# Optimization experiments

Hardware: AMD Instinct MI355X
Metric: run time of the kernel (lower is better)

Reference implementation:

```python
import jax, jax.numpy as jnp
import numpy as np

N_ENT = 50000
N_REL = 237
DIM = 200
BATCH = 1024
N_EDGE_RAW = 400000
WALK_LEN = 3


def _build_graph():
    rng = np.random.default_rng(0)
    src = rng.integers(0, N_ENT, N_EDGE_RAW)
    dst = rng.integers(0, N_ENT, N_EDGE_RAW)
    key = np.unique(src.astype(np.int64) * N_ENT + dst.astype(np.int64))
    row = (key // N_ENT).astype(np.int64)
    col = (key % N_ENT).astype(np.int64)
    # symmetric D^{-1/2} A D^{-1/2} normalization (binary coalesced adjacency)
    deg = np.bincount(row, minlength=N_ENT).astype(np.float64)
    dinv = np.where(deg > 0, deg ** -0.5, 0.0)
    adj_val = (dinv[row] * dinv[col]).astype(np.float32)
    # random walk of length 3 from every node (torch_cluster.random_walk semantics)
    rowptr = np.concatenate([[0], np.cumsum(np.bincount(row, minlength=N_ENT))]).astype(np.int64)
    cur = np.arange(N_ENT)
    walk = [cur]
    for _ in range(WALK_LEN):
        d = rowptr[cur + 1] - rowptr[cur]
        off = np.floor(rng.random(N_ENT) * np.maximum(d, 1)).astype(np.int64)
        idx = np.minimum(rowptr[cur] + off, len(row) - 1)
        nxt = np.where(d > 0, col[idx], cur)
        walk.append(nxt)
        cur = nxt
    walk = np.stack(walk, 1)  # (N, WALK_LEN+1)
    # scatter(rw_adj, 1, walk, 1): binary rows, duplicates collapse; then D^{-1} row-normalize
    rw_key = np.unique(np.repeat(np.arange(N_ENT), WALK_LEN + 1).astype(np.int64) * N_ENT + walk.reshape(-1))
    rw_row = (rw_key // N_ENT).astype(np.int64)
    rw_col = (rw_key % N_ENT).astype(np.int64)
    rw_deg = np.bincount(rw_row, minlength=N_ENT).astype(np.float64)
    rw_val = (1.0 / np.maximum(rw_deg[rw_row], 1.0)).astype(np.float32)
    return row, col, adj_val, rw_row, rw_col, rw_val


def setup_inputs() -> dict:
    row, col, adj_val, rw_row, rw_col, rw_val = _build_graph()
    E = row.shape[0]
    key = jax.random.key(0)
    ks = jax.random.split(key, 12)
    g = 0.05
    return dict(
        entity_emb=jax.random.normal(ks[0], (N_ENT, DIM), jnp.float32) * g,
        rel_emb=jax.random.normal(ks[1], (2 * N_REL, DIM * DIM), jnp.float32) * 0.01,
        node_W1=jax.random.normal(ks[2], (2, DIM, DIM), jnp.float32) * g,
        node_b1=jnp.zeros((2, DIM), jnp.float32),
        node_W2=jax.random.normal(ks[3], (2, DIM, 1), jnp.float32) * g,
        node_b2=jnp.zeros((2, 1), jnp.float32),
        edge_W1=jax.random.normal(ks[4], (2, 2 * DIM, DIM), jnp.float32) * g,
        edge_b1=jnp.zeros((2, DIM), jnp.float32),
        edge_W2=jax.random.normal(ks[5], (2, DIM, 1), jnp.float32) * g,
        edge_b2=jnp.zeros((2, 1), jnp.float32),
        adj_row=jnp.asarray(row), adj_col=jnp.asarray(col), adj_val=jnp.asarray(adj_val),
        rw_row=jnp.asarray(rw_row), rw_col=jnp.asarray(rw_col), rw_val=jnp.asarray(rw_val),
        node_eps=jax.random.uniform(ks[6], (2, N_ENT, 1), jnp.float32),
        edge_eps=jax.random.uniform(ks[7], (2, E, 1), jnp.float32),
        sub=jax.random.randint(ks[8], (BATCH,), 0, N_ENT),
        rel=jax.random.randint(ks[9], (BATCH,), 0, 2 * N_REL),
        obj=jax.random.randint(ks[10], (BATCH,), 0, N_ENT),
        neg_tail=jax.random.randint(ks[11], (BATCH, 2), 0, N_ENT),
    )


def _spmm(row, col, val, x, n):
    # sparse COO (row, col, val) @ dense x, output (n, d)
    return jax.ops.segment_sum(val[:, None] * x[col], row, num_segments=n)


def _gate(logits, u):
    # concrete-gate noise: eps ~ U(bias, 1-bias); sigmoid((logit(eps)+logits)/0.5)
    bias = 1e-4
    eps = (2.0 * bias - 1.0) * u + (1.0 - bias)
    return jax.nn.sigmoid((jnp.log(eps) - jnp.log1p(-eps) + logits) / 0.5)


def reference(entity_emb, rel_emb, node_W1, node_b1, node_W2, node_b2,
              edge_W1, edge_b1, edge_W2, edge_b2,
              adj_row, adj_col, adj_val, rw_row, rw_col, rw_val,
              node_eps, edge_eps, sub, rel, obj, neg_tail):
    n, d = entity_emb.shape
    e0 = entity_emb
    node_masks, edge_masks = [], []
    edge_cat = jnp.concatenate([e0[adj_row], e0[adj_col]], axis=-1)  # (E, 2d)
    for i in range(2):
        h = jax.nn.relu(e0 @ node_W1[i] + node_b1[i])
        node_masks.append(_gate(h @ node_W2[i] + node_b2[i], node_eps[i]))  # (n,1)
        he = jax.nn.relu(edge_cat @ edge_W1[i] + edge_b1[i])
        edge_masks.append(_gate(he @ edge_W2[i] + edge_b2[i], edge_eps[i])[:, 0])  # (E,)
    # node-drop branch: mix self vs random-walk mean-pooled, then GCN propagate
    x_nd = e0
    for i in range(2):
        mp = _spmm(rw_row, rw_col, rw_val, x_nd, n)
        x_nd = node_masks[i] * x_nd + (1.0 - node_masks[i]) * mp
        x_nd = _spmm(adj_row, adj_col, adj_val, x_nd, n)
    # edge-drop branch: rw propagation twice; only the LAST edge mask is applied (as in source)
    x_ed = e0
    new_edge = adj_val
    for i in range(2):
        x_ed = _spmm(rw_row, rw_col, rw_val, x_ed, n)
        new_edge = adj_val * edge_masks[i]
    x_ed = _spmm(adj_row, adj_col, new_edge, x_ed, n)
    # RESCAL scoring against all entities
    lhs1 = e0[sub]                                   # (B, d)
    rel1 = rel_emb[rel].reshape(-1, d, d)            # (B, d, d)
    self_hr = jnp.einsum('bd,bde->be', lhs1, rel1)   # (B, d)
    scores = jax.nn.sigmoid(self_hr @ e0.T)          # (B, n)
    return scores, x_nd, x_ed
```

## Files before the change

### kernel.cpp

```cpp
#include <hip/hip_runtime.h>
#include <math.h>

#define DIMV 200
typedef unsigned short ushort;
typedef unsigned int uint;
typedef __attribute__((ext_vector_type(8))) __bf16  bf16x8;
typedef __attribute__((ext_vector_type(4))) float   f32x4;

static __device__ __forceinline__ int lower_bound(const int* __restrict__ a, int n, int key) {
    int lo = 0, hi = n;
    while (lo < hi) {
        int mid = (lo + hi) >> 1;
        if (a[mid] < key) lo = mid + 1; else hi = mid;
    }
    return lo;
}

static __device__ __forceinline__ float gate_fn(float u, float logit) {
    float ee = fmaf(u, -0.9998f, 0.9999f);
    float g  = (logf(ee) - log1pf(-ee) + logit) * 2.0f;
    return 1.0f / (1.0f + expf(-g));
}

static __device__ __forceinline__ ushort f2bf(float f) {
    unsigned int u = __float_as_uint(f);
    return (ushort)((u + 0x7fffu + ((u >> 16) & 1u)) >> 16);
}
static __device__ __forceinline__ float2 bfp2f(uint u) {
    float2 r;
    r.x = __uint_as_float(u << 16);
    r.y = __uint_as_float(u & 0xffff0000u);
    return r;
}
static __device__ __forceinline__ uint f2bfp(float a, float b) {
    return (uint)f2bf(a) | ((uint)f2bf(b) << 16);
}

static __device__ __forceinline__ void cvt8_store(ushort* dst, const float* src) {
    float4 a = *(const float4*)src;
    float4 b = *(const float4*)(src + 4);
    dst[0] = f2bf(a.x); dst[1] = f2bf(a.y); dst[2] = f2bf(a.z); dst[3] = f2bf(a.w);
    dst[4] = f2bf(b.x); dst[5] = f2bf(b.y); dst[6] = f2bf(b.z); dst[7] = f2bf(b.w);
}
static __device__ __forceinline__ void zero8_store(ushort* dst) {
#pragma unroll
    for (int i = 0; i < 8; i++) dst[i] = 0;
}

__global__ __launch_bounds__(256) void prep_all(
    const float* __restrict__ e0, ushort* __restrict__ e0bf,
    const float* __restrict__ w1e_src, ushort* __restrict__ W1eT,
    const float* __restrict__ w1n_src, ushort* __restrict__ W1nT,
    const int* __restrict__ adj_row, int E, int* __restrict__ rp_adj,
    const int* __restrict__ rw_row, int Erw, int* __restrict__ rp_rw,
    const float* __restrict__ rel_emb, const int* __restrict__ sub,
    const int* __restrict__ rel, ushort* __restrict__ hrbf, int N)
{
    __shared__ float lhs[DIMV];
    int bid = blockIdx.x;
    const int t = threadIdx.x;

    const int NB0 = (N * 28 + 255) >> 8;
    if (bid < NB0) {
        int idx = bid * 256 + t;
        if (idx < N * 28) {
            int n = idx / 28, c = idx % 28;
            ushort* dst = e0bf + (size_t)n * 224 + c * 8;
            if (c < 25) cvt8_store(dst, e0 + (size_t)n * 200 + c * 8);
            else        zero8_store(dst);
        }
        return;
    }
    bid -= NB0;
    if (bid < 364) {
        int idx = bid * 256 + t;
        if (idx < 416 * 224) {
            int n = idx / 224, k = idx % 224;
            float v = 0.f;
            if (k < 200) {
                if (n < 200)      v = w1e_src[k * 200 + n];
                else if (n < 400) v = w1e_src[(k + 200) * 200 + (n - 200)];
            }
            W1eT[idx] = f2bf(v);
        }
        return;
    }
    bid -= 364;
    if (bid < 364) {
        int i = bid / 182;
        int idx = (bid % 182) * 256 + t;
        if (idx < 208 * 224) {
            int n = idx / 224, k = idx % 224;
            float v = (n < 200 && k < 200) ? w1n_src[i * 40000 + k * 200 + n] : 0.f;
            W1nT[(size_t)i * 208 * 224 + idx] = f2bf(v);
        }
        return;
    }
    bid -= 364;
    const int NBr = (N + 256) >> 8;
    if (bid < NBr) {
        int r = bid * 256 + t;
        if (r <= N) rp_adj[r] = lower_bound(adj_row, E, r);
        return;
    }
    bid -= NBr;
    if (bid < NBr) {
        int r = bid * 256 + t;
        if (r <= N) rp_rw[r] = lower_bound(rw_row, Erw, r);
        return;
    }
    bid -= NBr;
    {
        const int b = bid;
        if (t < DIMV) lhs[t] = e0[(size_t)sub[b] * DIMV + t];
        __syncthreads();
        if (t >= 224) return;
        if (t < DIMV) {
            const float* R = rel_emb + (size_t)rel[b] * (DIMV * DIMV);
            float acc = 0.f;
            for (int dd = 0; dd < DIMV; dd++)
                acc = fmaf(lhs[dd], R[dd * DIMV + t], acc);
            hrbf[(size_t)b * 224 + t] = f2bf(acc);
        } else {
            hrbf[(size_t)b * 224 + t] = 0;
        }
    }
}

__global__ __launch_bounds__(256) void fused_mlp(
    const ushort* __restrict__ e0bf, const ushort* __restrict__ W1eT,
    const ushort* __restrict__ W1nT, ushort* __restrict__ Pb,
    const float* __restrict__ nb1, const float* __restrict__ nW2,
    const float* __restrict__ nb2, const float* __restrict__ neps,
    float* __restrict__ node_mask, int N, int GX)
{
    __shared__ __align__(16) ushort As[2][128 * 40];
    __shared__ __align__(16) ushort Bs[2][208 * 40];
    __shared__ float bsh[208], wsh[208];

    const int r8  = blockIdx.x & 7;
    const int rem = blockIdx.x >> 3;
    const int y   = rem & 3;
    const int q4  = rem >> 2;
    const int x   = r8 + 8 * q4;
    if (x >= GX) return;

    const int t    = threadIdx.x;
    const int lane = t & 63;
    const int w    = t >> 6;
    const int q    = lane >> 4;
    const int ln   = lane & 15;
    const int r0   = x * 128;
    const bool edge = (y < 2);
    const int  i    = y - 2;
    const ushort* Wt = edge ? (W1eT + (size_t)y * 208 * 224)
                            : (W1nT + (size_t)i * 208 * 224);

    if (!edge && t < 208) {
        bsh[t] = (t < 200) ? nb1[i * 200 + t] : 0.f;
        wsh[t] = (t < 200) ? nW2[i * 200 + t] : 0.f;
    }

    f32x4 acc[2][13];
#pragma unroll
    for (int mt = 0; mt < 2; mt++)
#pragma unroll
        for (int nt = 0; nt < 13; nt++) {
            acc[mt][nt][0] = 0.f; acc[mt][nt][1] = 0.f;
            acc[mt][nt][2] = 0.f; acc[mt][nt][3] = 0.f;
        }

    auto stageA = [&](int ks, int buf) {
#pragma unroll
        for (int it = 0; it < 2; it++) {
            int f = t + it * 256;
            int m = f >> 2, c4 = f & 3;
            int g = r0 + m;
            ushort* dst = &As[buf][m * 40 + c4 * 8];
            if (g < N) *(bf16x8*)dst = *(const bf16x8*)&e0bf[(size_t)g * 224 + ks * 32 + c4 * 8];
            else       zero8_store(dst);
        }
    };
    auto stageB = [&](int ks, int buf) {
        for (int f = t; f < 832; f += 256) {
            int n = f >> 2, c4 = f & 3;
            *(bf16x8*)&Bs[buf][n * 40 + c4 * 8] =
                *(const bf16x8*)&Wt[(size_t)n * 224 + ks * 32 + c4 * 8];
        }
    };

    stageA(0, 0); stageB(0, 0);
    __syncthreads();

    for (int ks = 0; ks < 7; ks++) {
        int cur = ks & 1;
        if (ks + 1 < 7) { stageA(ks + 1, cur ^ 1); stageB(ks + 1, cur ^ 1); }
        bf16x8 af0 = *(const bf16x8*)&As[cur][(w * 32 + ln) * 40 + q * 8];
        bf16x8 af1 = *(const bf16x8*)&As[cur][(w * 32 + 16 + ln) * 40 + q * 8];
#pragma unroll
        for (int nt = 0; nt < 13; nt++) {
            bf16x8 bf = *(const bf16x8*)&Bs[cur][(nt * 16 + ln) * 40 + q * 8];
            acc[0][nt] = __builtin_amdgcn_mfma_f32_16x16x32_bf16(af0, bf, acc[0][nt], 0, 0, 0);
            acc[1][nt] = __builtin_amdgcn_mfma_f32_16x16x32_bf16(af1, bf, acc[1][nt], 0, 0, 0);
        }
        __syncthreads();
    }

    if (edge) {
#pragma unroll
        for (int mt = 0; mt < 2; mt++) {
            int gm = r0 + w * 32 + mt * 16 + q * 4;
#pragma unroll
            for (int nt = 0; nt < 13; nt++) {
                int gn = y * 208 + nt * 16 + ln;
                if (gn < 400) {
#pragma unroll
                    for (int r = 0; r < 4; r++)
                        if (gm + r < N) Pb[(size_t)(gm + r) * 400 + gn] = f2bf(acc[mt][nt][r]);
                }
            }
        }
    } else {
        float p[2][4];
#pragma unroll
        for (int mt = 0; mt < 2; mt++)
#pragma unroll
            for (int r = 0; r < 4; r++) {
                float s = 0.f;
#pragma unroll
                for (int nt = 0; nt < 13; nt++) {
                    int n = nt * 16 + ln;
                    float h = fmaxf(acc[mt][nt][r] + bsh[n], 0.f);
                    s = fmaf(h, wsh[n], s);
                }
                p[mt][r] = s;
            }
#pragma unroll
        for (int off = 1; off < 16; off <<= 1)
#pragma unroll
            for (int mt = 0; mt < 2; mt++)
#pragma unroll
                for (int r = 0; r < 4; r++)
                    p[mt][r] += __shfl_xor(p[mt][r], off);

        if (ln == 0) {
            float b2v = nb2[i];
            const float* epsi = neps + (size_t)i * N;
            float* outi = node_mask + (size_t)i * N;
#pragma unroll
            for (int mt = 0; mt < 2; mt++)
#pragma unroll
                for (int r = 0; r < 4; r++) {
                    int g = r0 + w * 32 + mt * 16 + q * 4 + r;
                    if (g < N) outi[g] = gate_fn(epsi[g], p[mt][r] + b2v);
                }
        }
    }
}

static __device__ __forceinline__ void spmm_bb_body(
    const uint* __restrict__ x, int xld, const int* __restrict__ rowptr,
    const int* __restrict__ col, const float* __restrict__ val,
    uint* __restrict__ out, int N, int bid, int t)
{
    const int sub = t >> 7;
    const int d2  = t & 127;
    const int r   = bid * 2 + sub;
    if (d2 >= 100 || r >= N) return;
    const int lo = rowptr[r], hi = rowptr[r + 1];
    float a0 = 0.f, a1 = 0.f, b0 = 0.f, b1 = 0.f;
    int e = lo;
    for (; e + 1 < hi; e += 2) {
        float2 xa = bfp2f(x[(size_t)col[e]     * xld + d2]);
        float2 xb = bfp2f(x[(size_t)col[e + 1] * xld + d2]);
        float v0 = val[e], v1 = val[e + 1];
        a0 = fmaf(v0, xa.x, a0); b0 = fmaf(v0, xa.y, b0);
        a1 = fmaf(v1, xb.x, a1); b1 = fmaf(v1, xb.y, b1);
    }
    if (e < hi) {
        float2 xa = bfp2f(x[(size_t)col[e] * xld + d2]);
        a0 = fmaf(val[e], xa.x, a0); b0 = fmaf(val[e], xa.y, b0);
    }
    out[(size_t)r * 100 + d2] = f2bfp(a0 + a1, b0 + b1);
}

__global__ __launch_bounds__(256) void k3_rw1_egate(
    const uint* __restrict__ e0u, const int* __restrict__ rp_rw,
    const int* __restrict__ rw_col, const float* __restrict__ rw_val,
    uint* __restrict__ Tb,
    const uint* __restrict__ P4, const int* __restrict__ rp_adj,
    const int* __restrict__ adj_col,
    const float* __restrict__ b1, const float* __restrict__ W2,
    const float* __restrict__ b2, const float* __restrict__ eps,
    float* __restrict__ edge_mask, int N, int NB_SP)
{
    int bid = blockIdx.x;
    const int t = threadIdx.x;
    if (bid < NB_SP) {
        spmm_bb_body(e0u, 112, rp_rw, rw_col, rw_val, Tb, N, bid, t);
        return;
    }
    bid -= NB_SP;
    const int lane = t & 63;
    const int w    = t >> 6;
    const int gw   = bid * 4 + w;
    const bool act1 = lane < 36;
    const int dA = 2 * lane;
    const int dB = 128 + 2 * lane;
    const float bb0x = b1[dA], bb0y = b1[dA + 1];
    const float ww0x = W2[dA], ww0y = W2[dA + 1];
    const float bb1x = act1 ? b1[dB] : 0.f, bb1y = act1 ? b1[dB + 1] : 0.f;
    const float ww1x = act1 ? W2[dB] : 0.f, ww1y = act1 ? W2[dB + 1] : 0.f;
    const float b2v = b2[0];

    const int r_lo = gw * 2;
    const int r_hi = min(r_lo + 2, N);
    for (int r = r_lo; r < r_hi; r++) {
        const uint* Pr = P4 + (size_t)r * 200;
        float2 a0 = bfp2f(Pr[lane]);
        float2 a1; a1.x = 0.f; a1.y = 0.f;
        if (act1) a1 = bfp2f(Pr[64 + lane]);
        a0.x += bb0x; a0.y += bb0y; a1.x += bb1x; a1.y += bb1y;
        const int lo = rp_adj[r], hi = rp_adj[r + 1];
        int e = lo;
        for (; e + 1 < hi; e += 2) {
            const uint* Pc0 = P4 + (size_t)adj_col[e]     * 200 + 100;
            const uint* Pc1 = P4 + (size_t)adj_col[e + 1] * 200 + 100;
            float2 q00 = bfp2f(Pc0[lane]);
            float2 q10 = bfp2f(Pc1[lane]);
            float2 q01, q11; q01.x = q01.y = q11.x = q11.y = 0.f;
            if (act1) { q01 = bfp2f(Pc0[64 + lane]); q11 = bfp2f(Pc1[64 + lane]); }
            float s0 = fmaxf(a0.x + q00.x, 0.f) * ww0x + fmaxf(a0.y + q00.y, 0.f) * ww0y
                     + fmaxf(a1.x + q01.x, 0.f) * ww1x + fmaxf(a1.y + q01.y, 0.f) * ww1y;
            float s1 = fmaxf(a0.x + q10.x, 0.f) * ww0x + fmaxf(a0.y + q10.y, 0.f) * ww0y
                     + fmaxf(a1.x + q11.x, 0.f) * ww1x + fmaxf(a1.y + q11.y, 0.f) * ww1y;
#pragma unroll
            for (int off = 32; off; off >>= 1) {
                s0 += __shfl_xor(s0, off);
                s1 += __shfl_xor(s1, off);
            }
            if (lane == 0) {
                edge_mask[e]     = gate_fn(eps[e],     s0 + b2v);
                edge_mask[e + 1] = gate_fn(eps[e + 1], s1 + b2v);
            }
        }
        if (e < hi) {
            const uint* Pc0 = P4 + (size_t)adj_col[e] * 200 + 100;
            float2 q00 = bfp2f(Pc0[lane]);
            float2 q01; q01.x = q01.y = 0.f;
            if (act1) q01 = bfp2f(Pc0[64 + lane]);
            float s0 = fmaxf(a0.x + q00.x, 0.f) * ww0x + fmaxf(a0.y + q00.y, 0.f) * ww0y
                     + fmaxf(a1.x + q01.x, 0.f) * ww1x + fmaxf(a1.y + q01.y, 0.f) * ww1y;
#pragma unroll
            for (int off = 32; off; off >>= 1) s0 += __shfl_xor(s0, off);
            if (lane == 0) edge_mask[e] = gate_fn(eps[e], s0 + b2v);
        }
    }
}

__global__ __launch_bounds__(256) void k4_rw2_combine(
    const uint* __restrict__ Tb, const int* __restrict__ rp_rw,
    const int* __restrict__ rw_col, const float* __restrict__ rw_val,
    uint* __restrict__ T2b,
    const float* __restrict__ e0, const float* __restrict__ mask,
    uint* __restrict__ xndb, int N, int NB_SP)
{
    int bid = blockIdx.x;
    const int t = threadIdx.x;
    if (bid < NB_SP) {
        spmm_bb_body(Tb, 100, rp_rw, rw_col, rw_val, T2b, N, bid, t);
        return;
    }
    bid -= NB_SP;
    int idx = bid * 256 + t;
    if (idx >= N * 100) return;
    float m = mask[idx / 100];
    float2 a = ((const float2*)e0)[idx];
    float2 b = bfp2f(Tb[idx]);
    xndb[idx] = f2bfp(fmaf(m, a.x - b.x, b.x), fmaf(m, a.y - b.y, b.y));
}

__global__ __launch_bounds__(256) void spmm_dual_bb(
    const uint* __restrict__ xA, const uint* __restrict__ xB,
    const int* __restrict__ rowptr, const int* __restrict__ col,
    const float* __restrict__ val, const float* __restrict__ emask,
    float* __restrict__ outA, uint* __restrict__ outB, int N)
{
    const int sub = threadIdx.x >> 7;
    const int d2  = threadIdx.x & 127;
    const int r   = blockIdx.x * 2 + sub;
    if (d2 >= 100 || r >= N) return;
    const int lo = rowptr[r], hi = rowptr[r + 1];
    float a0 = 0.f, a1 = 0.f, b0 = 0.f, b1 = 0.f;
    float c0 = 0.f, c1 = 0.f, d0 = 0.f, d1 = 0.f;
    int e = lo;
    for (; e + 1 < hi; e += 2) {
        size_t o0 = (size_t)col[e]     * 100 + d2;
        size_t o1 = (size_t)col[e + 1] * 100 + d2;
        float v0 = val[e], v1 = val[e + 1];
        float vm0 = v0 * emask[e], vm1 = v1 * emask[e + 1];
        float2 xa0 = bfp2f(xA[o0]), xa1 = bfp2f(xA[o1]);
        float2 xb0 = bfp2f(xB[o0]), xb1 = bfp2f(xB[o1]);
        a0 = fmaf(vm0, xa0.x, a0); b0 = fmaf(vm0, xa0.y, b0);
        a1 = fmaf(vm1, xa1.x, a1); b1 = fmaf(vm1, xa1.y, b1);
        c0 = fmaf(v0, xb0.x, c0);  d0 = fmaf(v0, xb0.y, d0);
        c1 = fmaf(v1, xb1.x, c1);  d1 = fmaf(v1, xb1.y, d1);
    }
    if (e < hi) {
        size_t o0 = (size_t)col[e] * 100 + d2;
        float v0 = val[e], vm0 = v0 * emask[e];
        float2 xa0 = bfp2f(xA[o0]);
        float2 xb0 = bfp2f(xB[o0]);
        a0 = fmaf(vm0, xa0.x, a0); b0 = fmaf(vm0, xa0.y, b0);
        c0 = fmaf(v0, xb0.x, c0);  d0 = fmaf(v0, xb0.y, d0);
    }
    float2 oA; oA.x = a0 + a1; oA.y = b0 + b1;
    ((float2*)outA)[(size_t)r * 100 + d2] = oA;
    outB[(size_t)r * 100 + d2] = f2bfp(c0 + c1, d0 + d1);
}

__global__ __launch_bounds__(256) void rw_combine_bb(
    const uint* __restrict__ x, const int* __restrict__ rowptr,
    const int* __restrict__ col, const float* __restrict__ val,
    const float* __restrict__ mask, uint* __restrict__ out, int N)
{
    const int sub = threadIdx.x >> 7;
    const int d2  = threadIdx.x & 127;
    const int r   = blockIdx.x * 2 + sub;
    if (d2 >= 100 || r >= N) return;
    const int lo = rowptr[r], hi = rowptr[r + 1];
    float a0 = 0.f, a1 = 0.f, b0 = 0.f, b1 = 0.f;
    int e = lo;
    for (; e + 1 < hi; e += 2) {
        float2 xa = bfp2f(x[(size_t)col[e]     * 100 + d2]);
        float2 xb = bfp2f(x[(size_t)col[e + 1] * 100 + d2]);
        float v0 = val[e], v1 = val[e + 1];
        a0 = fmaf(v0, xa.x, a0); b0 = fmaf(v0, xa.y, b0);
        a1 = fmaf(v1, xb.x, a1); b1 = fmaf(v1, xb.y, b1);
    }
    if (e < hi) {
        float2 xa = bfp2f(x[(size_t)col[e] * 100 + d2]);
        a0 = fmaf(val[e], xa.x, a0); b0 = fmaf(val[e], xa.y, b0);
    }
    const float m = mask[r];
    float2 xs = bfp2f(x[(size_t)r * 100 + d2]);
    float sx = a0 + a1, sy = b0 + b1;
    out[(size_t)r * 100 + d2] = f2bfp(fmaf(m, xs.x - sx, sx), fmaf(m, xs.y - sy, sy));
}

__global__ __launch_bounds__(256) void spmm_bf32(
    const uint* __restrict__ x, const int* __restrict__ rowptr,
    const int* __restrict__ col, const float* __restrict__ val,
    float* __restrict__ out, int N)
{
    const int sub = threadIdx.x >> 7;
    const int d2  = threadIdx.x & 127;
    const int r   = blockIdx.x * 2 + sub;
    if (d2 >= 100 || r >= N) return;
    const int lo = rowptr[r], hi = rowptr[r + 1];
    float a0 = 0.f, a1 = 0.f, b0 = 0.f, b1 = 0.f;
    int e = lo;
    for (; e + 1 < hi; e += 2) {
        float2 xa = bfp2f(x[(size_t)col[e]     * 100 + d2]);
        float2 xb = bfp2f(x[(size_t)col[e + 1] * 100 + d2]);
        float v0 = val[e], v1 = val[e + 1];
        a0 = fmaf(v0, xa.x, a0); b0 = fmaf(v0, xa.y, b0);
        a1 = fmaf(v1, xb.x, a1); b1 = fmaf(v1, xb.y, b1);
    }
    if (e < hi) {
        float2 xa = bfp2f(x[(size_t)col[e] * 100 + d2]);
        a0 = fmaf(val[e], xa.x, a0); b0 = fmaf(val[e], xa.y, b0);
    }
    float2 o; o.x = a0 + a1; o.y = b0 + b1;
    ((float2*)out)[(size_t)r * 100 + d2] = o;
}

__global__ __launch_bounds__(256) void scores_mfma(
    const ushort* __restrict__ hrbf, const ushort* __restrict__ e0bf,
    float* __restrict__ scores, int Nent, int GX)
{
    __shared__ __align__(16) ushort Bs[2][192 * 40];

    const int r8  = blockIdx.x & 7;
    const int rem = blockIdx.x >> 3;
    const int y   = rem & 7;
    const int q8  = rem >> 3;
    const int x   = r8 + 8 * q8;
    if (x >= GX) return;

    const int t    = threadIdx.x;
    const int lane = t & 63;
    const int w    = t >> 6;
    const int q    = lane >> 4;
    const int ln   = lane & 15;
    const int n0   = x * 192;
    const int b0   = y * 128;
    const int arow = b0 + w * 32 + ln;

    auto stageB = [&](int ks, int buf) {
        for (int f = t; f < 768; f += 256) {
            int n = f >> 2, c4 = f & 3;
            int gn = n0 + n;
            ushort* dst = &Bs[buf][n * 40 + c4 * 8];
            if (gn < Nent) *(bf16x8*)dst = *(const bf16x8*)&e0bf[(size_t)gn * 224 + ks * 32 + c4 * 8];
            else           zero8_store(dst);
        }
    };
    stageB(0, 0);

    f32x4 acc[2][12];
#pragma unroll
    for (int mt = 0; mt < 2; mt++)
#pragma unroll
        for (int nt = 0; nt < 12; nt++) {
            acc[mt][nt][0] = 0.f; acc[mt][nt][1] = 0.f;
            acc[mt][nt][2] = 0.f; acc[mt][nt][3] = 0.f;
        }

    bf16x8 a0 = *(const bf16x8*)&hrbf[(size_t)arow * 224 + q * 8];
    bf16x8 a1 = *(const bf16x8*)&hrbf[(size_t)(arow + 16) * 224 + q * 8];
    __syncthreads();

    for (int ks = 0; ks < 7; ks++) {
        int cur = ks & 1;
        bf16x8 a0n = a0, a1n = a1;
        if (ks + 1 < 7) {
            stageB(ks + 1, cur ^ 1);
            a0n = *(const bf16x8*)&hrbf[(size_t)arow * 224 + (ks + 1) * 32 + q * 8];
            a1n = *(const bf16x8*)&hrbf[(size_t)(arow + 16) * 224 + (ks + 1) * 32 + q * 8];
        }
#pragma unroll
        for (int nt = 0; nt < 12; nt++) {
            bf16x8 bf = *(const bf16x8*)&Bs[cur][(nt * 16 + ln) * 40 + q * 8];
            acc[0][nt] = __builtin_amdgcn_mfma_f32_16x16x32_bf16(a0, bf, acc[0][nt], 0, 0, 0);
            acc[1][nt] = __builtin_amdgcn_mfma_f32_16x16x32_bf16(a1, bf, acc[1][nt], 0, 0, 0);
        }
        __syncthreads();
        a0 = a0n; a1 = a1n;
    }

#pragma unroll
    for (int mt = 0; mt < 2; mt++) {
        int b = b0 + w * 32 + mt * 16 + q * 4;
#pragma unroll
        for (int nt = 0; nt < 12; nt++) {
            int n = n0 + nt * 16 + ln;
            if (n < Nent) {
#pragma unroll
                for (int r = 0; r < 4; r++)
                    scores[(size_t)(b + r) * Nent + n] = 1.f / (1.f + __expf(-acc[mt][nt][r]));
            }
        }
    }
}

extern "C" void kernel_launch(void* const* d_in, const int* in_sizes, int n_in,
                              void* d_out, int out_size, void* d_ws, size_t ws_size,
                              hipStream_t stream)
{
    const float* e0       = (const float*)d_in[0];
    const float* rel_emb  = (const float*)d_in[1];
    const float* node_W1  = (const float*)d_in[2];
    const float* node_b1  = (const float*)d_in[3];
    const float* node_W2  = (const float*)d_in[4];
    const float* node_b2  = (const float*)d_in[5];
    const float* edge_W1  = (const float*)d_in[6];
    const float* edge_b1  = (const float*)d_in[7];
    const float* edge_W2  = (const float*)d_in[8];
    const float* edge_b2  = (const float*)d_in[9];
    const int*   adj_row  = (const int*)d_in[10];
    const int*   adj_col  = (const int*)d_in[11];
    const float* adj_val  = (const float*)d_in[12];
    const int*   rw_row   = (const int*)d_in[13];
    const int*   rw_col   = (const int*)d_in[14];
    const float* rw_val   = (const float*)d_in[15];
    const float* node_eps = (const float*)d_in[16];
    const float* edge_eps = (const float*)d_in[17];
    const int*   sub      = (const int*)d_in[18];
    const int*   rel      = (const int*)d_in[19];

    const int E   = in_sizes[10];
    const int Erw = in_sizes[13];
    const int N   = in_sizes[0] / DIMV;
    const int B   = in_sizes[18];

    ushort* W1eT = (ushort*)d_ws;
    ushort* W1nT = W1eT + 416 * 224;
    ushort* e0bf = W1nT + 2 * 208 * 224;
    ushort* hrbf = e0bf + (size_t)N * 224;
    float*  fb   = (float*)(hrbf + (size_t)B * 224);
    float*  node_mask = fb;
    float*  edge_mask = node_mask + 2 * (size_t)N;
    int*    rp_adj = (int*)(edge_mask + E);
    int*    rp_rw  = rp_adj + (N + 1);

    float* out    = (float*)d_out;
    float* scores = out;
    float* x_nd   = out + (size_t)B * N;
    float* x_ed   = x_nd + (size_t)N * DIMV;
    uint*   Tb   = (uint*)scores;
    uint*   T2b  = Tb   + (size_t)N * 100;
    uint*   xndb = T2b  + (size_t)N * 100;
    uint*   Tnb  = xndb + (size_t)N * 100;
    uint*   Pb   = Tnb  + (size_t)N * 100;

    const int NB_SP = (N + 1) / 2;
    const int NB0   = (N * 28 + 255) / 256;
    const int NBr   = (N + 256) / 256;
    const int prep_blocks = NB0 + 364 + 364 + NBr + NBr + B;
    const int GXg = (N + 127) / 128;
    const int GXs = (N + 191) / 192;

    prep_all<<<prep_blocks, 256, 0, stream>>>(
        e0, e0bf, edge_W1 + 400 * 200, W1eT, node_W1, W1nT,
        adj_row, E, rp_adj, rw_row, Erw, rp_rw,
        rel_emb, sub, rel, hrbf, N);

    fused_mlp<<<32 * ((GXg + 7) / 8), 256, 0, stream>>>(
        e0bf, W1eT, W1nT, (ushort*)Pb,
        node_b1, node_W2, node_b2, node_eps, node_mask, N, GXg);

    k3_rw1_egate<<<NB_SP + (NB_SP + 3) / 4, 256, 0, stream>>>(
        (const uint*)e0bf, rp_rw, rw_col, rw_val, Tb,
        Pb, rp_adj, adj_col,
        edge_b1 + 200, edge_W2 + 200, edge_b2 + 1, edge_eps + (size_t)E,
        edge_mask, N, NB_SP);

    k4_rw2_combine<<<NB_SP + (N * 100 + 255) / 256, 256, 0, stream>>>(
        Tb, rp_rw, rw_col, rw_val, T2b, e0, node_mask, xndb, N, NB_SP);

    spmm_dual_bb<<<NB_SP, 256, 0, stream>>>(
        T2b, xndb, rp_adj, adj_col, adj_val, edge_mask, x_ed, Tnb, N);

    rw_combine_bb<<<NB_SP, 256, 0, stream>>>(
        Tnb, rp_rw, rw_col, rw_val, node_mask + N, T2b, N);

    spmm_bf32<<<NB_SP, 256, 0, stream>>>(T2b, rp_adj, adj_col, adj_val, x_nd, N);

    scores_mfma<<<64 * ((GXs + 7) / 8), 256, 0, stream>>>(
        hrbf, e0bf, scores, N, GXs);
}
```

Before: 936.6 us.

## Fuse sparse propagation stages into one cooperative kernel with grid syncs

Replaces the five separate sparse-stage kernel launches with a single persistent cooperative kernel that loops over virtual blocks and separates stages with grid-wide syncs, keeping the old kernels as a fallback if the cooperative launch fails. The SpMM and edge-gate loops are also unrolled from 2 to 4 edges, with four independent accumulators to expose more memory-level parallelism. The aim is to cut launch gaps and tail effects between dependent stages. In exchange, the grid is capped at occupancy-limited residency, grid.sync adds its own cost, and the wider unroll raises register pressure.

```diff
diff --git a/kernel.cpp b/kernel.cpp
--- a/kernel.cpp
+++ b/kernel.cpp
@@ -1,5 +1,8 @@
 #include <hip/hip_runtime.h>
+#include <hip/hip_cooperative_groups.h>
 #include <math.h>
+
+namespace cg = cooperative_groups;
 
 #define DIMV 200
 typedef unsigned short ushort;
@@ -261,58 +264,153 @@
 static __device__ __forceinline__ void spmm_bb_body(
     const uint* __restrict__ x, int xld, const int* __restrict__ rowptr,
     const int* __restrict__ col, const float* __restrict__ val,
-    uint* __restrict__ out, int N, int bid, int t)
-{
-    const int sub = t >> 7;
-    const int d2  = t & 127;
-    const int r   = bid * 2 + sub;
+    uint* __restrict__ out, int N, int vb, int t)
+{
+    const int half = t >> 7;
+    const int d2   = t & 127;
+    const int r    = vb * 2 + half;
     if (d2 >= 100 || r >= N) return;
     const int lo = rowptr[r], hi = rowptr[r + 1];
-    float a0 = 0.f, a1 = 0.f, b0 = 0.f, b1 = 0.f;
+    float ax0=0.f,ay0=0.f,ax1=0.f,ay1=0.f,ax2=0.f,ay2=0.f,ax3=0.f,ay3=0.f;
     int e = lo;
-    for (; e + 1 < hi; e += 2) {
-        float2 xa = bfp2f(x[(size_t)col[e]     * xld + d2]);
-        float2 xb = bfp2f(x[(size_t)col[e + 1] * xld + d2]);
-        float v0 = val[e], v1 = val[e + 1];
-        a0 = fmaf(v0, xa.x, a0); b0 = fmaf(v0, xa.y, b0);
-        a1 = fmaf(v1, xb.x, a1); b1 = fmaf(v1, xb.y, b1);
-    }
-    if (e < hi) {
-        float2 xa = bfp2f(x[(size_t)col[e] * xld + d2]);
-        a0 = fmaf(val[e], xa.x, a0); b0 = fmaf(val[e], xa.y, b0);
-    }
-    out[(size_t)r * 100 + d2] = f2bfp(a0 + a1, b0 + b1);
-}
-
-__global__ __launch_bounds__(256) void k3_rw1_egate(
-    const uint* __restrict__ e0u, const int* __restrict__ rp_rw,
-    const int* __restrict__ rw_col, const float* __restrict__ rw_val,
-    uint* __restrict__ Tb,
-    const uint* __restrict__ P4, const int* __restrict__ rp_adj,
-    const int* __restrict__ adj_col,
-    const float* __restrict__ b1, const float* __restrict__ W2,
-    const float* __restrict__ b2, const float* __restrict__ eps,
-    float* __restrict__ edge_mask, int N, int NB_SP)
-{
-    int bid = blockIdx.x;
-    const int t = threadIdx.x;
-    if (bid < NB_SP) {
-        spmm_bb_body(e0u, 112, rp_rw, rw_col, rw_val, Tb, N, bid, t);
-        return;
-    }
-    bid -= NB_SP;
+    for (; e + 3 < hi; e += 4) {
+        int c0=col[e], c1=col[e+1], c2=col[e+2], c3=col[e+3];
+        float v0=val[e], v1=val[e+1], v2=val[e+2], v3=val[e+3];
+        float2 f0=bfp2f(x[(size_t)c0*xld+d2]);
+        float2 f1=bfp2f(x[(size_t)c1*xld+d2]);
+        float2 f2=bfp2f(x[(size_t)c2*xld+d2]);
+        float2 f3=bfp2f(x[(size_t)c3*xld+d2]);
+        ax0=fmaf(v0,f0.x,ax0); ay0=fmaf(v0,f0.y,ay0);
+        ax1=fmaf(v1,f1.x,ax1); ay1=fmaf(v1,f1.y,ay1);
+        ax2=fmaf(v2,f2.x,ax2); ay2=fmaf(v2,f2.y,ay2);
+        ax3=fmaf(v3,f3.x,ax3); ay3=fmaf(v3,f3.y,ay3);
+    }
+    for (; e < hi; e++) {
+        float2 f0=bfp2f(x[(size_t)col[e]*xld+d2]);
+        ax0=fmaf(val[e],f0.x,ax0); ay0=fmaf(val[e],f0.y,ay0);
+    }
+    out[(size_t)r*100+d2] = f2bfp((ax0+ax1)+(ax2+ax3), (ay0+ay1)+(ay2+ay3));
+}
+
+static __device__ __forceinline__ void dual_body(
+    const uint* __restrict__ xA, const uint* __restrict__ xB,
+    const int* __restrict__ rowptr, const int* __restrict__ col,
+    const float* __restrict__ val, const float* __restrict__ emask,
+    float* __restrict__ outA, uint* __restrict__ outB, int N, int vb, int t)
+{
+    const int half = t >> 7;
+    const int d2   = t & 127;
+    const int r    = vb * 2 + half;
+    if (d2 >= 100 || r >= N) return;
+    const int lo = rowptr[r], hi = rowptr[r + 1];
+    float ax0=0.f,ay0=0.f,ax1=0.f,ay1=0.f,ax2=0.f,ay2=0.f,ax3=0.f,ay3=0.f;
+    float cx0=0.f,cy0=0.f,cx1=0.f,cy1=0.f,cx2=0.f,cy2=0.f,cx3=0.f,cy3=0.f;
+    int e = lo;
+    for (; e + 3 < hi; e += 4) {
+        size_t o0=(size_t)col[e]*100+d2,   o1=(size_t)col[e+1]*100+d2;
+        size_t o2=(size_t)col[e+2]*100+d2, o3=(size_t)col[e+3]*100+d2;
+        float v0=val[e], v1=val[e+1], v2=val[e+2], v3=val[e+3];
+        float m0=v0*emask[e], m1=v1*emask[e+1], m2=v2*emask[e+2], m3=v3*emask[e+3];
+        float2 a0=bfp2f(xA[o0]), a1=bfp2f(xA[o1]), a2=bfp2f(xA[o2]), a3=bfp2f(xA[o3]);
+        float2 b0=bfp2f(xB[o0]), b1=bfp2f(xB[o1]), b2=bfp2f(xB[o2]), b3=bfp2f(xB[o3]);
+        ax0=fmaf(m0,a0.x,ax0); ay0=fmaf(m0,a0.y,ay0);
+        ax1=fmaf(m1,a1.x,ax1); ay1=fmaf(m1,a1.y,ay1);
+        ax2=fmaf(m2,a2.x,ax2); ay2=fmaf(m2,a2.y,ay2);
+        ax3=fmaf(m3,a3.x,ax3); ay3=fmaf(m3,a3.y,ay3);
+        cx0=fmaf(v0,b0.x,cx0); cy0=fmaf(v0,b0.y,cy0);
+        cx1=fmaf(v1,b1.x,cx1); cy1=fmaf(v1,b1.y,cy1);
+        cx2=fmaf(v2,b2.x,cx2); cy2=fmaf(v2,b2.y,cy2);
+        cx3=fmaf(v3,b3.x,cx3); cy3=fmaf(v3,b3.y,cy3);
+    }
+    for (; e < hi; e++) {
+        size_t o0=(size_t)col[e]*100+d2;
+        float v0=val[e], m0=v0*emask[e];
+        float2 a0=bfp2f(xA[o0]); float2 b0=bfp2f(xB[o0]);
+        ax0=fmaf(m0,a0.x,ax0); ay0=fmaf(m0,a0.y,ay0);
+        cx0=fmaf(v0,b0.x,cx0); cy0=fmaf(v0,b0.y,cy0);
+    }
+    float2 oA; oA.x=(ax0+ax1)+(ax2+ax3); oA.y=(ay0+ay1)+(ay2+ay3);
+    ((float2*)outA)[(size_t)r*100+d2] = oA;
+    outB[(size_t)r*100+d2] = f2bfp((cx0+cx1)+(cx2+cx3), (cy0+cy1)+(cy2+cy3));
+}
+
+static __device__ __forceinline__ void rwcomb_body(
+    const uint* __restrict__ x, const int* __restrict__ rowptr,
+    const int* __restrict__ col, const float* __restrict__ val,
+    const float* __restrict__ mask, uint* __restrict__ out, int N, int vb, int t)
+{
+    const int half = t >> 7;
+    const int d2   = t & 127;
+    const int r    = vb * 2 + half;
+    if (d2 >= 100 || r >= N) return;
+    const int lo = rowptr[r], hi = rowptr[r + 1];
+    float ax0=0.f,ay0=0.f,ax1=0.f,ay1=0.f,ax2=0.f,ay2=0.f,ax3=0.f,ay3=0.f;
+    int e = lo;
+    for (; e + 3 < hi; e += 4) {
+        int c0=col[e], c1=col[e+1], c2=col[e+2], c3=col[e+3];
+        float v0=val[e], v1=val[e+1], v2=val[e+2], v3=val[e+3];
+        float2 f0=bfp2f(x[(size_t)c0*100+d2]);
+        float2 f1=bfp2f(x[(size_t)c1*100+d2]);
+        float2 f2=bfp2f(x[(size_t)c2*100+d2]);
+        float2 f3=bfp2f(x[(size_t)c3*100+d2]);
+        ax0=fmaf(v0,f0.x,ax0); ay0=fmaf(v0,f0.y,ay0);
+        ax1=fmaf(v1,f1.x,ax1); ay1=fmaf(v1,f1.y,ay1);
+        ax2=fmaf(v2,f2.x,ax2); ay2=fmaf(v2,f2.y,ay2);
+        ax3=fmaf(v3,f3.x,ax3); ay3=fmaf(v3,f3.y,ay3);
+    }
+    for (; e < hi; e++) {
+        float2 f0=bfp2f(x[(size_t)col[e]*100+d2]);
+        ax0=fmaf(val[e],f0.x,ax0); ay0=fmaf(val[e],f0.y,ay0);
+    }
+    const float m = mask[r];
+    float2 xs = bfp2f(x[(size_t)r*100+d2]);
+    float sx=(ax0+ax1)+(ax2+ax3), sy=(ay0+ay1)+(ay2+ay3);
+    out[(size_t)r*100+d2] = f2bfp(fmaf(m, xs.x-sx, sx), fmaf(m, xs.y-sy, sy));
+}
+
+static __device__ __forceinline__ void bf32_body(
+    const uint* __restrict__ x, const int* __restrict__ rowptr,
+    const int* __restrict__ col, const float* __restrict__ val,
+    float* __restrict__ out, int N, int vb, int t)
+{
+    const int half = t >> 7;
+    const int d2   = t & 127;
+    const int r    = vb * 2 + half;
+    if (d2 >= 100 || r >= N) return;
+    const int lo = rowptr[r], hi = rowptr[r + 1];
+    float ax0=0.f,ay0=0.f,ax1=0.f,ay1=0.f,ax2=0.f,ay2=0.f,ax3=0.f,ay3=0.f;
+    int e = lo;
+    for (; e + 3 < hi; e += 4) {
+        int c0=col[e], c1=col[e+1], c2=col[e+2], c3=col[e+3];
+        float v0=val[e], v1=val[e+1], v2=val[e+2], v3=val[e+3];
+        float2 f0=bfp2f(x[(size_t)c0*100+d2]);
+        float2 f1=bfp2f(x[(size_t)c1*100+d2]);
+        float2 f2=bfp2f(x[(size_t)c2*100+d2]);
+        float2 f3=bfp2f(x[(size_t)c3*100+d2]);
+        ax0=fmaf(v0,f0.x,ax0); ay0=fmaf(v0,f0.y,ay0);
+        ax1=fmaf(v1,f1.x,ax1); ay1=fmaf(v1,f1.y,ay1);
+        ax2=fmaf(v2,f2.x,ax2); ay2=fmaf(v2,f2.y,ay2);
+        ax3=fmaf(v3,f3.x,ax3); ay3=fmaf(v3,f3.y,ay3);
+    }
+    for (; e < hi; e++) {
+        float2 f0=bfp2f(x[(size_t)col[e]*100+d2]);
+        ax0=fmaf(val[e],f0.x,ax0); ay0=fmaf(val[e],f0.y,ay0);
+    }
+    float2 o; o.x=(ax0+ax1)+(ax2+ax3); o.y=(ay0+ay1)+(ay2+ay3);
+    ((float2*)out)[(size_t)r*100+d2] = o;
+}
+
+static __device__ __forceinline__ void egate_body(
+    int vb, int t, const uint* __restrict__ P4, const int* __restrict__ rp_adj,
+    const int* __restrict__ adj_col, const float* __restrict__ eps,
+    float* __restrict__ edge_mask, int N,
+    float bb0x, float bb0y, float bb1x, float bb1y,
+    float ww0x, float ww0y, float ww1x, float ww1y, float b2v)
+{
     const int lane = t & 63;
     const int w    = t >> 6;
-    const int gw   = bid * 4 + w;
+    const int gw   = vb * 4 + w;
     const bool act1 = lane < 36;
-    const int dA = 2 * lane;
-    const int dB = 128 + 2 * lane;
-    const float bb0x = b1[dA], bb0y = b1[dA + 1];
-    const float ww0x = W2[dA], ww0y = W2[dA + 1];
-    const float bb1x = act1 ? b1[dB] : 0.f, bb1y = act1 ? b1[dB + 1] : 0.f;
-    const float ww1x = act1 ? W2[dB] : 0.f, ww1y = act1 ? W2[dB + 1] : 0.f;
-    const float b2v = b2[0];
-
     const int r_lo = gw * 2;
     const int r_hi = min(r_lo + 2, N);
     for (int r = r_lo; r < r_hi; r++) {
@@ -323,34 +421,44 @@
         a0.x += bb0x; a0.y += bb0y; a1.x += bb1x; a1.y += bb1y;
         const int lo = rp_adj[r], hi = rp_adj[r + 1];
         int e = lo;
-        for (; e + 1 < hi; e += 2) {
-            const uint* Pc0 = P4 + (size_t)adj_col[e]     * 200 + 100;
-            const uint* Pc1 = P4 + (size_t)adj_col[e + 1] * 200 + 100;
-            float2 q00 = bfp2f(Pc0[lane]);
-            float2 q10 = bfp2f(Pc1[lane]);
-            float2 q01, q11; q01.x = q01.y = q11.x = q11.y = 0.f;
-            if (act1) { q01 = bfp2f(Pc0[64 + lane]); q11 = bfp2f(Pc1[64 + lane]); }
-            float s0 = fmaxf(a0.x + q00.x, 0.f) * ww0x + fmaxf(a0.y + q00.y, 0.f) * ww0y
-                     + fmaxf(a1.x + q01.x, 0.f) * ww1x + fmaxf(a1.y + q01.y, 0.f) * ww1y;
-            float s1 = fmaxf(a0.x + q10.x, 0.f) * ww0x + fmaxf(a0.y + q10.y, 0.f) * ww0y
-                     + fmaxf(a1.x + q11.x, 0.f) * ww1x + fmaxf(a1.y + q11.y, 0.f) * ww1y;
+        for (; e + 3 < hi; e += 4) {
+            const uint* c0 = P4 + (size_t)adj_col[e]     * 200 + 100;
+            const uint* c1 = P4 + (size_t)adj_col[e + 1] * 200 + 100;
+            const uint* c2 = P4 + (size_t)adj_col[e + 2] * 200 + 100;
+            const uint* c3 = P4 + (size_t)adj_col[e + 3] * 200 + 100;
+            float2 q0l=bfp2f(c0[lane]), q1l=bfp2f(c1[lane]),
+                   q2l=bfp2f(c2[lane]), q3l=bfp2f(c3[lane]);
+            float2 q0h,q1h,q2h,q3h;
+            q0h.x=q0h.y=q1h.x=q1h.y=q2h.x=q2h.y=q3h.x=q3h.y=0.f;
+            if (act1) {
+                q0h=bfp2f(c0[64+lane]); q1h=bfp2f(c1[64+lane]);
+                q2h=bfp2f(c2[64+lane]); q3h=bfp2f(c3[64+lane]);
+            }
+            float s0 = fmaxf(a0.x+q0l.x,0.f)*ww0x + fmaxf(a0.y+q0l.y,0.f)*ww0y
+                     + fmaxf(a1.x+q0h.x,0.f)*ww1x + fmaxf(a1.y+q0h.y,0.f)*ww1y;
+            float s1 = fmaxf(a0.x+q1l.x,0.f)*ww0x + fmaxf(a0.y+q1l.y,0.f)*ww0y
+                     + fmaxf(a1.x+q1h.x,0.f)*ww1x + fmaxf(a1.y+q1h.y,0.f)*ww1y;
+            float s2 = fmaxf(a0.x+q2l.x,0.f)*ww0x + fmaxf(a0.y+q2l.y,0.f)*ww0y
+                     + fmaxf(a1.x+q2h.x,0.f)*ww1x + fmaxf(a1.y+q2h.y,0.f)*ww1y;
+            float s3 = fmaxf(a0.x+q3l.x,0.f)*ww0x + fmaxf(a0.y+q3l.y,0.f)*ww0y
+                     + fmaxf(a1.x+q3h.x,0.f)*ww1x + fmaxf(a1.y+q3h.y,0.f)*ww1y;
 #pragma unroll
             for (int off = 32; off; off >>= 1) {
-                s0 += __shfl_xor(s0, off);
-                s1 += __shfl_xor(s1, off);
+                s0 += __shfl_xor(s0, off); s1 += __shfl_xor(s1, off);
+                s2 += __shfl_xor(s2, off); s3 += __shfl_xor(s3, off);
             }
-            if (lane == 0) {
-                edge_mask[e]     = gate_fn(eps[e],     s0 + b2v);
-                edge_mask[e + 1] = gate_fn(eps[e + 1], s1 + b2v);
+            if (lane < 4) {
+                float sv = (lane == 0) ? s0 : (lane == 1) ? s1 : (lane == 2) ? s2 : s3;
+                edge_mask[e + lane] = gate_fn(eps[e + lane], sv + b2v);
             }
         }
-        if (e < hi) {
-            const uint* Pc0 = P4 + (size_t)adj_col[e] * 200 + 100;
-            float2 q00 = bfp2f(Pc0[lane]);
-            float2 q01; q01.x = q01.y = 0.f;
-            if (act1) q01 = bfp2f(Pc0[64 + lane]);
-            float s0 = fmaxf(a0.x + q00.x, 0.f) * ww0x + fmaxf(a0.y + q00.y, 0.f) * ww0y
-                     + fmaxf(a1.x + q01.x, 0.f) * ww1x + fmaxf(a1.y + q01.y, 0.f) * ww1y;
+        for (; e < hi; e++) {
+            const uint* c0 = P4 + (size_t)adj_col[e] * 200 + 100;
+            float2 q0l = bfp2f(c0[lane]);
+            float2 q0h; q0h.x = q0h.y = 0.f;
+            if (act1) q0h = bfp2f(c0[64 + lane]);
+            float s0 = fmaxf(a0.x+q0l.x,0.f)*ww0x + fmaxf(a0.y+q0l.y,0.f)*ww0y
+                     + fmaxf(a1.x+q0h.x,0.f)*ww1x + fmaxf(a1.y+q0h.y,0.f)*ww1y;
 #pragma unroll
             for (int off = 32; off; off >>= 1) s0 += __shfl_xor(s0, off);
             if (lane == 0) edge_mask[e] = gate_fn(eps[e], s0 + b2v);
@@ -358,21 +466,90 @@
     }
 }
 
-__global__ __launch_bounds__(256) void k4_rw2_combine(
+__global__ __launch_bounds__(256) void sparse_coop(
+    const uint* e0u, const int* rp_rw, const int* rw_col, const float* rw_val,
+    uint* Tb, const uint* P4, const int* rp_adj, const int* adj_col,
+    const float* adj_val, const float* eb1, const float* eW2, const float* eb2,
+    const float* eeps, float* edge_mask, const float* e0,
+    const float* node_mask, uint* T2b, uint* xndb, uint* Tnb,
+    float* x_ed, float* x_nd, int N, int NB_SP, int EGB, int CB)
+{
+    cg::grid_group grid = cg::this_grid();
+    const int t  = threadIdx.x;
+    const int nb = gridDim.x;
+    const int lane = t & 63;
+    const bool act1 = lane < 36;
+    const int dA = 2 * lane, dB = 128 + 2 * lane;
+    const float bb0x = eb1[dA],  bb0y = eb1[dA + 1];
+    const float ww0x = eW2[dA],  ww0y = eW2[dA + 1];
+    const float bb1x = act1 ? eb1[dB] : 0.f, bb1y = act1 ? eb1[dB + 1] : 0.f;
+    const float ww1x = act1 ? eW2[dB] : 0.f, ww1y = act1 ? eW2[dB + 1] : 0.f;
+    const float b2v = eb2[0];
+
+    for (int vb = blockIdx.x; vb < NB_SP + EGB; vb += nb) {
+        if (vb < NB_SP) spmm_bb_body(e0u, 112, rp_rw, rw_col, rw_val, Tb, N, vb, t);
+        else egate_body(vb - NB_SP, t, P4, rp_adj, adj_col, eeps, edge_mask, N,
+                        bb0x, bb0y, bb1x, bb1y, ww0x, ww0y, ww1x, ww1y, b2v);
+    }
+    __threadfence(); grid.sync();
+
+    for (int vb = blockIdx.x; vb < NB_SP + CB; vb += nb) {
+        if (vb < NB_SP) spmm_bb_body(Tb, 100, rp_rw, rw_col, rw_val, T2b, N, vb, t);
+        else {
+            int idx = (vb - NB_SP) * 256 + t;
+            if (idx < N * 100) {
+                float m = node_mask[idx / 100];
+                float2 a = ((const float2*)e0)[idx];
+                float2 b = bfp2f(Tb[idx]);
+                xndb[idx] = f2bfp(fmaf(m, a.x - b.x, b.x), fmaf(m, a.y - b.y, b.y));
+            }
+        }
+    }
+    __threadfence(); grid.sync();
+
+    for (int vb = blockIdx.x; vb < NB_SP; vb += nb)
+        dual_body(T2b, xndb, rp_adj, adj_col, adj_val, edge_mask, x_ed, Tnb, N, vb, t);
+    __threadfence(); grid.sync();
+
+    for (int vb = blockIdx.x; vb < NB_SP; vb += nb)
+        rwcomb_body(Tnb, rp_rw, rw_col, rw_val, node_mask + N, T2b, N, vb, t);
+    __threadfence(); grid.sync();
+
+    for (int vb = blockIdx.x; vb < NB_SP; vb += nb)
+        bf32_body(T2b, rp_adj, adj_col, adj_val, x_nd, N, vb, t);
+}
+
+__global__ __launch_bounds__(256) void fb_rw1_egate(
+    const uint* __restrict__ e0u, const int* __restrict__ rp_rw,
+    const int* __restrict__ rw_col, const float* __restrict__ rw_val,
+    uint* __restrict__ Tb, const uint* __restrict__ P4,
+    const int* __restrict__ rp_adj, const int* __restrict__ adj_col,
+    const float* __restrict__ eb1, const float* __restrict__ eW2,
+    const float* __restrict__ eb2, const float* __restrict__ eeps,
+    float* __restrict__ edge_mask, int N, int NB_SP)
+{
+    int bid = blockIdx.x;
+    const int t = threadIdx.x;
+    if (bid < NB_SP) { spmm_bb_body(e0u, 112, rp_rw, rw_col, rw_val, Tb, N, bid, t); return; }
+    const int lane = t & 63;
+    const bool act1 = lane < 36;
+    const int dA = 2 * lane, dB = 128 + 2 * lane;
+    egate_body(bid - NB_SP, t, P4, rp_adj, adj_col, eeps, edge_mask, N,
+               eb1[dA], eb1[dA + 1], act1 ? eb1[dB] : 0.f, act1 ? eb1[dB + 1] : 0.f,
+               eW2[dA], eW2[dA + 1], act1 ? eW2[dB] : 0.f, act1 ? eW2[dB + 1] : 0.f,
+               eb2[0]);
+}
+
+__global__ __launch_bounds__(256) void fb_rw2_combine(
     const uint* __restrict__ Tb, const int* __restrict__ rp_rw,
     const int* __restrict__ rw_col, const float* __restrict__ rw_val,
-    uint* __restrict__ T2b,
-    const float* __restrict__ e0, const float* __restrict__ mask,
-    uint* __restrict__ xndb, int N, int NB_SP)
+    uint* __restrict__ T2b, const float* __restrict__ e0,
+    const float* __restrict__ mask, uint* __restrict__ xndb, int N, int NB_SP)
 {
     int bid = blockIdx.x;
     const int t = threadIdx.x;
-    if (bid < NB_SP) {
-        spmm_bb_body(Tb, 100, rp_rw, rw_col, rw_val, T2b, N, bid, t);
-        return;
-    }
-    bid -= NB_SP;
-    int idx = bid * 256 + t;
+    if (bid < NB_SP) { spmm_bb_body(Tb, 100, rp_rw, rw_col, rw_val, T2b, N, bid, t); return; }
+    int idx = (bid - NB_SP) * 256 + t;
     if (idx >= N * 100) return;
     float m = mask[idx / 100];
     float2 a = ((const float2*)e0)[idx];
@@ -380,99 +557,29 @@
     xndb[idx] = f2bfp(fmaf(m, a.x - b.x, b.x), fmaf(m, a.y - b.y, b.y));
 }
 
-__global__ __launch_bounds__(256) void spmm_dual_bb(
+__global__ __launch_bounds__(256) void fb_dual(
     const uint* __restrict__ xA, const uint* __restrict__ xB,
     const int* __restrict__ rowptr, const int* __restrict__ col,
     const float* __restrict__ val, const float* __restrict__ emask,
     float* __restrict__ outA, uint* __restrict__ outB, int N)
 {
-    const int sub = threadIdx.x >> 7;
-    const int d2  = threadIdx.x & 127;
-    const int r   = blockIdx.x * 2 + sub;
-    if (d2 >= 100 || r >= N) return;
-    const int lo = rowptr[r], hi = rowptr[r + 1];
-    float a0 = 0.f, a1 = 0.f, b0 = 0.f, b1 = 0.f;
-    float c0 = 0.f, c1 = 0.f, d0 = 0.f, d1 = 0.f;
-    int e = lo;
-    for (; e + 1 < hi; e += 2) {
-        size_t o0 = (size_t)col[e]     * 100 + d2;
-        size_t o1 = (size_t)col[e + 1] * 100 + d2;
-        float v0 = val[e], v1 = val[e + 1];
-        float vm0 = v0 * emask[e], vm1 = v1 * emask[e + 1];
-        float2 xa0 = bfp2f(xA[o0]), xa1 = bfp2f(xA[o1]);
-        float2 xb0 = bfp2f(xB[o0]), xb1 = bfp2f(xB[o1]);
-        a0 = fmaf(vm0, xa0.x, a0); b0 = fmaf(vm0, xa0.y, b0);
-        a1 = fmaf(vm1, xa1.x, a1); b1 = fmaf(vm1, xa1.y, b1);
-        c0 = fmaf(v0, xb0.x, c0);  d0 = fmaf(v0, xb0.y, d0);
-        c1 = fmaf(v1, xb1.x, c1);  d1 = fmaf(v1, xb1.y, d1);
-    }
-    if (e < hi) {
-        size_t o0 = (size_t)col[e] * 100 + d2;
-        float v0 = val[e], vm0 = v0 * emask[e];
-        float2 xa0 = bfp2f(xA[o0]);
-        float2 xb0 = bfp2f(xB[o0]);
-        a0 = fmaf(vm0, xa0.x, a0); b0 = fmaf(vm0, xa0.y, b0);
-        c0 = fmaf(v0, xb0.x, c0);  d0 = fmaf(v0, xb0.y, d0);
-    }
-    float2 oA; oA.x = a0 + a1; oA.y = b0 + b1;
-    ((float2*)outA)[(size_t)r * 100 + d2] = oA;
-    outB[(size_t)r * 100 + d2] = f2bfp(c0 + c1, d0 + d1);
-}
-
-__global__ __launch_bounds__(256) void rw_combine_bb(
+    dual_body(xA, xB, rowptr, col, val, emask, outA, outB, N, blockIdx.x, threadIdx.x);
+}
+
+__global__ __launch_bounds__(256) void fb_rwcomb(
     const uint* __restrict__ x, const int* __restrict__ rowptr,
     const int* __restrict__ col, const float* __restrict__ val,
     const float* __restrict__ mask, uint* __restrict__ out, int N)
 {
-    const int sub = threadIdx.x >> 7;
-    const int d2  = threadIdx.x & 127;
-    const int r   = blockIdx.x * 2 + sub;
-    if (d2 >= 100 || r >= N) return;
-    const int lo = rowptr[r], hi = rowptr[r + 1];
-    float a0 = 0.f, a1 = 0.f, b0 = 0.f, b1 = 0.f;
-    int e = lo;
-    for (; e + 1 < hi; e += 2) {
-        float2 xa = bfp2f(x[(size_t)col[e]     * 100 + d2]);
-        float2 xb = bfp2f(x[(size_t)col[e + 1] * 100 + d2]);
-        float v0 = val[e], v1 = val[e + 1];
-        a0 = fmaf(v0, xa.x, a0); b0 = fmaf(v0, xa.y, b0);
-        a1 = fmaf(v1, xb.x, a1); b1 = fmaf(v1, xb.y, b1);
-    }
-    if (e < hi) {
-        float2 xa = bfp2f(x[(size_t)col[e] * 100 + d2]);
-        a0 = fmaf(val[e], xa.x, a0); b0 = fmaf(val[e], xa.y, b0);
-    }
-    const float m = mask[r];
-    float2 xs = bfp2f(x[(size_t)r * 100 + d2]);
-    float sx = a0 + a1, sy = b0 + b1;
-    out[(size_t)r * 100 + d2] = f2bfp(fmaf(m, xs.x - sx, sx), fmaf(m, xs.y - sy, sy));
-}
-
-__global__ __launch_bounds__(256) void spmm_bf32(
+    rwcomb_body(x, rowptr, col, val, mask, out, N, blockIdx.x, threadIdx.x);
+}
+
+__global__ __launch_bounds__(256) void fb_bf32(
     const uint* __restrict__ x, const int* __restrict__ rowptr,
     const int* __restrict__ col, const float* __restrict__ val,
     float* __restrict__ out, int N)
 {
-    const int sub = threadIdx.x >> 7;
-    const int d2  = threadIdx.x & 127;
-    const int r   = blockIdx.x * 2 + sub;
-    if (d2 >= 100 || r >= N) return;
-    const int lo = rowptr[r], hi = rowptr[r + 1];
-    float a0 = 0.f, a1 = 0.f, b0 = 0.f, b1 = 0.f;
-    int e = lo;
-    for (; e + 1 < hi; e += 2) {
-        float2 xa = bfp2f(x[(size_t)col[e]     * 100 + d2]);
-        float2 xb = bfp2f(x[(size_t)col[e + 1] * 100 + d2]);
-        float v0 = val[e], v1 = val[e + 1];
-        a0 = fmaf(v0, xa.x, a0); b0 = fmaf(v0, xa.y, b0);
-        a1 = fmaf(v1, xb.x, a1); b1 = fmaf(v1, xb.y, b1);
-    }
-    if (e < hi) {
-        float2 xa = bfp2f(x[(size_t)col[e] * 100 + d2]);
-        a0 = fmaf(val[e], xa.x, a0); b0 = fmaf(val[e], xa.y, b0);
-    }
-    float2 o; o.x = a0 + a1; o.y = b0 + b1;
-    ((float2*)out)[(size_t)r * 100 + d2] = o;
+    bf32_body(x, rowptr, col, val, out, N, blockIdx.x, threadIdx.x);
 }
 
 __global__ __launch_bounds__(256) void scores_mfma(
@@ -605,6 +712,8 @@
     uint*   Pb   = Tnb  + (size_t)N * 100;
 
     const int NB_SP = (N + 1) / 2;
+    const int EGB   = (N + 7) / 8;
+    const int CB    = (N * 100 + 255) / 256;
     const int NB0   = (N * 28 + 255) / 256;
     const int NBr   = (N + 256) / 256;
     const int prep_blocks = NB0 + 364 + 364 + NBr + NBr + B;
@@ -620,22 +729,51 @@
         e0bf, W1eT, W1nT, (ushort*)Pb,
         node_b1, node_W2, node_b2, node_eps, node_mask, N, GXg);
 
-    k3_rw1_egate<<<NB_SP + (NB_SP + 3) / 4, 256, 0, stream>>>(
-        (const uint*)e0bf, rp_rw, rw_col, rw_val, Tb,
-        Pb, rp_adj, adj_col,
-        edge_b1 + 200, edge_W2 + 200, edge_b2 + 1, edge_eps + (size_t)E,
-        edge_mask, N, NB_SP);
-
-    k4_rw2_combine<<<NB_SP + (N * 100 + 255) / 256, 256, 0, stream>>>(
-        Tb, rp_rw, rw_col, rw_val, T2b, e0, node_mask, xndb, N, NB_SP);
-
-    spmm_dual_bb<<<NB_SP, 256, 0, stream>>>(
-        T2b, xndb, rp_adj, adj_col, adj_val, edge_mask, x_ed, Tnb, N);
-
-    rw_combine_bb<<<NB_SP, 256, 0, stream>>>(
-        Tnb, rp_rw, rw_col, rw_val, node_mask + N, T2b, N);
-
-    spmm_bf32<<<NB_SP, 256, 0, stream>>>(T2b, rp_adj, adj_col, adj_val, x_nd, N);
+    static int coop_blocks = -2;
+    if (coop_blocks == -2) {
+        int nb = 0;
+        if (hipOccupancyMaxActiveBlocksPerMultiprocessor(
+                &nb, (const void*)sparse_coop, 256, 0) == hipSuccess && nb >= 1)
+            coop_blocks = nb * 256;
+        else
+            coop_blocks = -1;
+    }
+
+    const uint*  e0u_  = (const uint*)e0bf;
+    const uint*  P4_   = Pb;
+    const float* eb1_  = edge_b1 + 200;
+    const float* eW2_  = edge_W2 + 200;
+    const float* eb2_  = edge_b2 + 1;
+    const float* eeps_ = edge_eps + (size_t)E;
+    int N_ = N, NBSP_ = NB_SP, EGB_ = EGB, CB_ = CB;
+
+    bool coop_done = false;
+    if (coop_blocks > 0) {
+        void* args[] = {
+            (void*)&e0u_, (void*)&rp_rw, (void*)&rw_col, (void*)&rw_val,
+            (void*)&Tb, (void*)&P4_, (void*)&rp_adj, (void*)&adj_col,
+            (void*)&adj_val, (void*)&eb1_, (void*)&eW2_, (void*)&eb2_,
+            (void*)&eeps_, (void*)&edge_mask, (void*)&e0,
+            (void*)&node_mask, (void*)&T2b, (void*)&xndb, (void*)&Tnb,
+            (void*)&x_ed, (void*)&x_nd, (void*)&N_, (void*)&NBSP_,
+            (void*)&EGB_, (void*)&CB_ };
+        hipError_t le = hipLaunchCooperativeKernel(
+            (const void*)sparse_coop, dim3(coop_blocks), dim3(256), args, 0, stream);
+        if (le == hipSuccess) coop_done = true;
+        else (void)hipGetLastError();
+    }
+    if (!coop_done) {
+        fb_rw1_egate<<<NB_SP + EGB, 256, 0, stream>>>(
+            e0u_, rp_rw, rw_col, rw_val, Tb, P4_, rp_adj, adj_col,
+            eb1_, eW2_, eb2_, eeps_, edge_mask, N, NB_SP);
+        fb_rw2_combine<<<NB_SP + CB, 256, 0, stream>>>(
+            Tb, rp_rw, rw_col, rw_val, T2b, e0, node_mask, xndb, N, NB_SP);
+        fb_dual<<<NB_SP, 256, 0, stream>>>(
+            T2b, xndb, rp_adj, adj_col, adj_val, edge_mask, x_ed, Tnb, N);
+        fb_rwcomb<<<NB_SP, 256, 0, stream>>>(
+            Tnb, rp_rw, rw_col, rw_val, node_mask + N, T2b, N);
+        fb_bf32<<<NB_SP, 256, 0, stream>>>(T2b, rp_adj, adj_col, adj_val, x_nd, N);
+    }
 
     scores_mfma<<<64 * ((GXs + 7) / 8), 256, 0, stream>>>(
         hrbf, e0bf, scores, N, GXs);
```

Measured after the change: 1.719 ms. 1.84x slower.
